# Optimization experiments

Measured on AMD Instinct MI355X. Metric: run time of the kernel, lower is better.

## Reference

```python
import jax, jax.numpy as jnp
import numpy as np

THRESHOLD = 0.5

def _conv(x, w, b):
    y = jax.lax.conv_general_dilated(x, w, (1, 1), 'SAME',
                                     dimension_numbers=('NCHW', 'OIHW', 'NCHW'))
    return y + b[None, :, None, None]

def _gather2d(img, iy, ix):
    # img [B,C,H,W], iy/ix [B,h,w] int -> [B,C,h,w]
    return jax.vmap(lambda im, y, x: im[:, y, x])(img, iy, ix)

def _grid_sample_bilinear(img, grid):
    # torch F.grid_sample(mode='bilinear', padding_mode='border', align_corners=False)
    # img [B,C,H,W], grid [B,h,w,2] with (x,y) in [-1,1]
    B, C, H, W = img.shape
    x = (grid[..., 0] + 1.0) * (W * 0.5) - 0.5
    y = (grid[..., 1] + 1.0) * (H * 0.5) - 0.5
    x0 = jnp.floor(x); y0 = jnp.floor(y)
    wx = (x - x0)[:, None, :, :]; wy = (y - y0)[:, None, :, :]
    x0i = jnp.clip(x0.astype(jnp.int32), 0, W - 1)
    x1i = jnp.clip(x0.astype(jnp.int32) + 1, 0, W - 1)
    y0i = jnp.clip(y0.astype(jnp.int32), 0, H - 1)
    y1i = jnp.clip(y0.astype(jnp.int32) + 1, 0, H - 1)
    v00 = _gather2d(img, y0i, x0i); v01 = _gather2d(img, y0i, x1i)
    v10 = _gather2d(img, y1i, x0i); v11 = _gather2d(img, y1i, x1i)
    return (v00 * (1 - wx) * (1 - wy) + v01 * wx * (1 - wy)
            + v10 * (1 - wx) * wy + v11 * wx * wy)

def _encoder(lr, w_in, b_in, res_w, res_b):
    x = _conv(lr, w_in, b_in)
    for i in range(res_w.shape[0]):  # small fixed layer count
        r = _conv(jax.nn.relu(_conv(x, res_w[i, 0], res_b[i, 0])), res_w[i, 1], res_b[i, 1])
        x = x + r
    return x  # [B,64,Hl,Wl]

def _make_inp(feat, coord, cell):
    # nearest-sampled feature + relative coord + scaled cell (LIIF-style make_inp)
    B, C, Hl, Wl = feat.shape
    y = (coord[..., 0] + 1.0) * (Hl * 0.5) - 0.5
    x = (coord[..., 1] + 1.0) * (Wl * 0.5) - 0.5
    iyn = jnp.clip(jnp.floor(y + 0.5).astype(jnp.int32), 0, Hl - 1)
    ixn = jnp.clip(jnp.floor(x + 0.5).astype(jnp.int32), 0, Wl - 1)
    fs = _gather2d(feat, iyn, ixn).transpose(0, 2, 3, 1)  # [B,h,w,C]
    cy = (2.0 * iyn + 1.0) / Hl - 1.0
    cx = (2.0 * ixn + 1.0) / Wl - 1.0
    rel = jnp.stack([(coord[..., 0] - cy) * Hl, (coord[..., 1] - cx) * Wl], axis=-1)
    cell_s = cell * jnp.array([Hl, Wl], dtype=cell.dtype)
    return jnp.concatenate([fs, rel, cell_s], axis=-1)  # [B,h,w,C+4]

def setup_inputs() -> dict:
    key = jax.random.key(0)
    ks = jax.random.split(key, 16)
    B, Hl, Wl, h, w, C = 2, 96, 96, 384, 384, 64
    lr = jax.random.normal(ks[0], (B, 3, Hl, Wl), jnp.float32)
    ys = (jnp.arange(h, dtype=jnp.float32) + 0.5) / h * 2.0 - 1.0
    xs = (jnp.arange(w, dtype=jnp.float32) + 0.5) / w * 2.0 - 1.0
    gy, gx = jnp.meshgrid(ys, xs, indexing='ij')
    coord = jnp.broadcast_to(jnp.stack([gy, gx], -1), (B, h, w, 2))  # (y,x)
    cell = jnp.broadcast_to(jnp.array([2.0 / h, 2.0 / w], jnp.float32), (B, h, w, 2))
    def lin(k, fan_in, shape):
        return jax.random.normal(k, shape, jnp.float32) / np.sqrt(fan_in)
    D = C + 4  # 68
    return {
        'lr': lr, 'coord': coord, 'cell': cell,
        'enc_w_in': jax.random.normal(ks[1], (C, 3, 3, 3), jnp.float32) * 0.05,
        'enc_b_in': jnp.zeros((C,), jnp.float32),
        'enc_res_w': jax.random.normal(ks[2], (4, 2, C, C, 3, 3), jnp.float32) * 0.02,
        'enc_res_b': jnp.zeros((4, 2, C), jnp.float32),
        'cls_w1': lin(ks[3], D, (D, 64)), 'cls_b1': jnp.zeros((64,), jnp.float32),
        'cls_w2': lin(ks[4], 64, (64, 2)), 'cls_b2': jnp.zeros((2,), jnp.float32),
        'lw1': lin(ks[5], D, (D, 64)), 'lb1': jnp.zeros((64,), jnp.float32),
        'lw2': lin(ks[6], 64, (64, 64)), 'lb2': jnp.zeros((64,), jnp.float32),
        'lw3': lin(ks[7], 64, (64, 3)), 'lb3': jnp.zeros((3,), jnp.float32),
        'hw1': lin(ks[8], D, (D, 256)), 'hb1': jnp.zeros((256,), jnp.float32),
        'hmid_w': lin(ks[9], 256, (2, 256, 256)), 'hmid_b': jnp.zeros((2, 256), jnp.float32),
        'hw_out': lin(ks[10], 256, (256, 3)), 'hb_out': jnp.zeros((3,), jnp.float32),
    }

def reference(lr, coord, cell, enc_w_in, enc_b_in, enc_res_w, enc_res_b,
              cls_w1, cls_b1, cls_w2, cls_b2,
              lw1, lb1, lw2, lb2, lw3, lb3,
              hw1, hb1, hmid_w, hmid_b, hw_out, hb_out):
    feat = _encoder(lr, enc_w_in, enc_b_in, enc_res_w, enc_res_b)
    inp = _make_inp(feat, coord, cell)  # [B,h,w,68]
    # classifier -> softmax difficulty gate
    logits = jax.nn.relu(inp @ cls_w1 + cls_b1) @ cls_w2 + cls_b2
    diff = jax.nn.softmax(logits, axis=-1)
    hard = diff[..., 1] > THRESHOLD  # [B,h,w]
    # light sampler (dense over all pixels; where-select == gather/scatter dispatch)
    pl = jax.nn.relu(inp @ lw1 + lb1)
    pl = jax.nn.relu(pl @ lw2 + lb2)
    pl = pl @ lw3 + lb3
    # heavy sampler
    ph = jax.nn.relu(inp @ hw1 + hb1)
    for i in range(hmid_w.shape[0]):
        ph = jax.nn.relu(ph @ hmid_w[i] + hmid_b[i])
    ph = ph @ hw_out + hb_out
    pred = jnp.where(hard[..., None], ph, pl)  # [B,h,w,3]
    pred = pred.transpose(0, 3, 1, 2)  # [B,3,h,w]
    pred = pred + _grid_sample_bilinear(lr, coord[..., ::-1])  # coord.flip(-1) -> (x,y)
    ratio_easy = jnp.mean(1.0 - hard.astype(jnp.float32))
    return (pred, ratio_easy)
```

## Files before the change

### kernel.cpp

```cpp
#include <hip/hip_runtime.h>

#define HL 96
#define WL 96
#define HO 384
#define WO 384
#define NPIX (2*HO*WO)
#define FEAT_ELEMS ((size_t)2*64*HL*WL)
#define PLANE (HL*WL)

typedef unsigned short us4 __attribute__((ext_vector_type(4)));
typedef unsigned short us8 __attribute__((ext_vector_type(8)));
typedef __bf16         b8  __attribute__((ext_vector_type(8)));
typedef float          f32x4 __attribute__((ext_vector_type(4)));

__device__ __forceinline__ unsigned short f2b(float x) {
  unsigned u = __builtin_bit_cast(unsigned, x);
  unsigned r = (u + 0x7FFFu + ((u >> 16) & 1u)) >> 16;
  return (unsigned short)r;
}

__device__ __forceinline__ f32x4 MF(us8 a, us8 b, f32x4 c) {
  return __builtin_amdgcn_mfma_f32_16x16x32_bf16(
      __builtin_bit_cast(b8, a), __builtin_bit_cast(b8, b), c, 0, 0, 0);
}

template<int CIN, int COPT, bool RELU, bool RES>
__global__ __launch_bounds__(256) void conv_s_k(
    const float* __restrict__ in, const float* __restrict__ wP,
    const float* __restrict__ bias, const float* __restrict__ res,
    float* __restrict__ out)
{
  const int t   = threadIdx.x;
  const int p   = blockIdx.x * 256 + t;
  const int co0 = blockIdx.y * COPT;
  const int b   = blockIdx.z;
  const int x   = p % WL;
  const bool xl = (x == 0), xr = (x == WL - 1);

  float acc[COPT];
  #pragma unroll
  for (int j = 0; j < COPT; ++j) acc[j] = bias[co0 + j];

  int  ic[3]; bool yv[3];
  int  im[3], ip[3];
  #pragma unroll
  for (int ky = 0; ky < 3; ++ky) {
    int pr = p + (ky - 1) * WL;
    yv[ky] = ((unsigned)pr < (unsigned)PLANE);
    ic[ky] = yv[ky] ? pr : 0;
    im[ky] = ic[ky] - 1; if (im[ky] < 0) im[ky] = 0;
    ip[ky] = ic[ky] + 1; if (ip[ky] > PLANE - 1) ip[ky] = PLANE - 1;
  }

  const float* inb = in + (size_t)b * CIN * PLANE;

  #pragma unroll 2
  for (int ci = 0; ci < CIN; ++ci) {
    const float* pl = inb + (size_t)ci * PLANE;
    #pragma unroll
    for (int ky = 0; ky < 3; ++ky) {
      float am = pl[im[ky]];
      float a0 = pl[ic[ky]];
      float ap = pl[ip[ky]];
      if (!yv[ky]) { am = 0.f; a0 = 0.f; ap = 0.f; }
      if (xl) am = 0.f;
      if (xr) ap = 0.f;
      const float* wrow = wP + (size_t)(ci * 9 + ky * 3) * 64 + co0;
      #pragma unroll
      for (int j = 0; j < COPT; ++j) acc[j] += am * wrow[j];
      #pragma unroll
      for (int j = 0; j < COPT; ++j) acc[j] += a0 * wrow[64 + j];
      #pragma unroll
      for (int j = 0; j < COPT; ++j) acc[j] += ap * wrow[128 + j];
    }
  }

  size_t ob = ((size_t)b * 64 + co0) * PLANE + p;
  #pragma unroll
  for (int j = 0; j < COPT; ++j) {
    float v = acc[j];
    if (RELU) v = fmaxf(v, 0.f);
    if (RES)  v += res[ob + (size_t)j * PLANE];
    out[ob + (size_t)j * PLANE] = v;
  }
}

__device__ __forceinline__ void prep_bf16(const float* __restrict__ src,
    unsigned short* __restrict__ dst, int K, int N, int Kp, int i)
{
  int n = i / Kp, k = i - n * Kp;
  float v = (k < K && n < N) ? src[(size_t)k * N + n] : 0.f;
  dst[i] = f2b(v);
}
__device__ __forceinline__ void prep_conv(const float* __restrict__ src,
    float* __restrict__ dst, int cin, int i)
{
  int co = i % 64; int r = i / 64;
  int ci = r / 9, tap = r % 9;
  dst[i] = src[((size_t)co * cin + ci) * 9 + tap];
}

#define PREP_TOTAL 467648
__global__ __launch_bounds__(256) void prep_all_k(
    const float* __restrict__ lw1, const float* __restrict__ lw2,
    const float* __restrict__ lw3, const float* __restrict__ hw1,
    const float* __restrict__ hmw, const float* __restrict__ hwo,
    const float* __restrict__ enc_w_in, const float* __restrict__ enc_rw,
    unsigned short* __restrict__ lw1T, unsigned short* __restrict__ lw2T,
    unsigned short* __restrict__ lw3T, unsigned short* __restrict__ hw1T,
    unsigned short* __restrict__ hm0T, unsigned short* __restrict__ hm1T,
    unsigned short* __restrict__ hwoT, float* __restrict__ cwIn,
    float* __restrict__ cwRes)
{
  int i = blockIdx.x * 256 + threadIdx.x;
  if (i >= PREP_TOTAL) return;
  if (i < 6144)  { prep_bf16(lw1, lw1T, 68, 64, 96, i);    return; } i -= 6144;
  if (i < 4096)  { prep_bf16(lw2, lw2T, 64, 64, 64, i);    return; } i -= 4096;
  if (i < 1024)  { prep_bf16(lw3, lw3T, 64, 3, 64, i);     return; } i -= 1024;
  if (i < 24576) { prep_bf16(hw1, hw1T, 68, 256, 96, i);   return; } i -= 24576;
  if (i < 65536) { prep_bf16(hmw, hm0T, 256, 256, 256, i); return; } i -= 65536;
  if (i < 65536) { prep_bf16(hmw + 65536, hm1T, 256, 256, 256, i); return; } i -= 65536;
  if (i < 4096)  { prep_bf16(hwo, hwoT, 256, 3, 256, i);   return; } i -= 4096;
  if (i < 1728)  { prep_conv(enc_w_in, cwIn, 3, i);        return; } i -= 1728;
  int l = i / 36864, r = i % 36864;
  prep_conv(enc_rw + (size_t)l * 36864, cwRes + (size_t)l * 36864, 64, r);
}

__global__ __launch_bounds__(256) void nchw_to_nhwc_k(const float* __restrict__ in,
                                                      float* __restrict__ out)
{
  __shared__ float s[64][65];
  const int b = blockIdx.y;
  const int pix0 = blockIdx.x * 64;
  const int t = threadIdx.x;
  #pragma unroll
  for (int cc = 0; cc < 16; ++cc) {
    int co = cc * 4 + (t >> 6);
    int px = t & 63;
    s[px][co] = in[((size_t)b * 64 + co) * PLANE + pix0 + px];
  }
  __syncthreads();
  #pragma unroll
  for (int pp = 0; pp < 16; ++pp) {
    int px = pp * 4 + (t >> 6);
    int co = t & 63;
    out[((size_t)b * PLANE + pix0 + px) * 64 + co] = s[px][co];
  }
}

template<int NT, int KT>
__device__ __forceinline__ void mfma_compute(
    const unsigned short* __restrict__ aBase, int AS,
    const unsigned short* __restrict__ WT, int Kpad,
    int n0, int lane, f32x4 (&acc)[4][NT])
{
  const int lr = lane & 15;
  const int lc = lane >> 4;
  #pragma unroll
  for (int m = 0; m < 4; ++m)
    #pragma unroll
    for (int j = 0; j < NT; ++j) acc[m][j] = (f32x4){0.f, 0.f, 0.f, 0.f};

  const unsigned short* aP = aBase + lr * AS + lc * 8;
  const unsigned short* bP = WT + (size_t)(n0 + lr) * Kpad + lc * 8;

  constexpr int KCH = (KT >= 4) ? 4 : KT;
  #pragma unroll
  for (int kc = 0; kc < KT; kc += KCH) {
    us8 breg[KCH][NT];
    #pragma unroll
    for (int kk = 0; kk < KCH; ++kk)
      #pragma unroll
      for (int j = 0; j < NT; ++j)
        breg[kk][j] = *(const us8*)(bP + (size_t)j * 16 * Kpad + (kc + kk) * 32);
    #pragma unroll
    for (int kc2 = 0; kc2 < KCH; ++kc2) {
      us8 a0[4];
      #pragma unroll
      for (int m = 0; m < 4; ++m)
        a0[m] = *(const us8*)(aP + (m * 16) * AS + (kc + kc2) * 32);
      #pragma unroll
      for (int m = 0; m < 4; ++m)
        #pragma unroll
        for (int j = 0; j < NT; ++j)
          acc[m][j] = MF(a0[m], breg[kc2][j], acc[m][j]);
    }
  }
}

template<int NT, bool RELU>
__device__ __forceinline__ void mfma_store(
    const f32x4 (&acc)[4][NT], const float* __restrict__ bias,
    unsigned short* __restrict__ dBase, int DS, int dCol0, int n0, int lane)
{
  const int lr = lane & 15;
  const int lc = lane >> 4;
  #pragma unroll
  for (int j = 0; j < NT; ++j) {
    int n = n0 + j * 16 + lr;
    float bv = bias[n];
    #pragma unroll
    for (int m = 0; m < 4; ++m)
      #pragma unroll
      for (int r = 0; r < 4; ++r) {
        float v = acc[m][j][r] + bv;
        if (RELU) v = fmaxf(v, 0.f);
        dBase[(m * 16 + lc * 4 + r) * DS + dCol0 + n] = f2b(v);
      }
  }
}

template<int KT>
__device__ __forceinline__ void mfma_out3w(
    const unsigned short* __restrict__ aBase, int AS,
    const unsigned short* __restrict__ WT, int Kpad,
    const float* __restrict__ bias, float (*dst)[4], int mtile, int lane)
{
  const int lr = lane & 15;
  const int lc = lane >> 4;
  f32x4 acc = (f32x4){0.f, 0.f, 0.f, 0.f};
  const unsigned short* aP = aBase + (mtile * 16 + lr) * AS + lc * 8;
  const unsigned short* bP = WT + (size_t)lr * Kpad + lc * 8;

  constexpr int KCH = (KT >= 4) ? 4 : KT;
  #pragma unroll
  for (int kc = 0; kc < KT; kc += KCH) {
    us8 breg[KCH];
    #pragma unroll
    for (int kk = 0; kk < KCH; ++kk)
      breg[kk] = *(const us8*)(bP + (kc + kk) * 32);
    #pragma unroll
    for (int kk = 0; kk < KCH; ++kk) {
      us8 a = *(const us8*)(aP + (kc + kk) * 32);
      acc = MF(a, breg[kk], acc);
    }
  }
  if (lr < 3) {
    float bv = bias[lr];
    #pragma unroll
    for (int r = 0; r < 4; ++r)
      dst[mtile * 16 + lc * 4 + r][lr] = acc[r] + bv;
  }
}

__device__ __forceinline__ void nearest_idx(float gy, float gx, int& iy, int& ix)
{
  float fy = (gy + 1.f) * (HL * 0.5f) - 0.5f;
  float fx = (gx + 1.f) * (WL * 0.5f) - 0.5f;
  iy = min(max((int)floorf(fy + 0.5f), 0), HL - 1);
  ix = min(max((int)floorf(fx + 0.5f), 0), WL - 1);
}

__device__ __forceinline__ float bilinear_lr(const float* __restrict__ lrimg,
                                             int b, int ch, float gy, float gx)
{
  float x = (gx + 1.f) * (WL * 0.5f) - 0.5f;
  float y = (gy + 1.f) * (HL * 0.5f) - 0.5f;
  float xf = floorf(x), yf = floorf(y);
  float wx = x - xf, wy = y - yf;
  int x0i = min(max((int)xf,     0), WL - 1);
  int x1i = min(max((int)xf + 1, 0), WL - 1);
  int y0i = min(max((int)yf,     0), HL - 1);
  int y1i = min(max((int)yf + 1, 0), HL - 1);
  const float* img = lrimg + ((size_t)b * 3 + ch) * PLANE;
  float v00 = img[y0i * WL + x0i], v01 = img[y0i * WL + x1i];
  float v10 = img[y1i * WL + x0i], v11 = img[y1i * WL + x1i];
  return v00 * (1.f - wx) * (1.f - wy) + v01 * wx * (1.f - wy)
       + v10 * (1.f - wx) * wy + v11 * wx * wy;
}

template<int JB>
__device__ __forceinline__ void cls_block2(
    const float* __restrict__ fpA, const float* __restrict__ fpB,
    const float4& eA, const float4& eB,
    const float* __restrict__ cw1, const float* __restrict__ cb1,
    const float* __restrict__ cw2, int j0,
    float& l0a, float& l1a, float& l0b, float& l1b)
{
  float accA[JB], accB[JB];
  #pragma unroll
  for (int j = 0; j < JB; ++j) { accA[j] = cb1[j0 + j]; accB[j] = accA[j]; }
  #pragma unroll 4
  for (int kq = 0; kq < 16; ++kq) {
    float4 a4A = *(const float4*)(fpA + kq * 4);
    float4 a4B = *(const float4*)(fpB + kq * 4);
    float avA[4] = {a4A.x, a4A.y, a4A.z, a4A.w};
    float avB[4] = {a4B.x, a4B.y, a4B.z, a4B.w};
    #pragma unroll
    for (int kk = 0; kk < 4; ++kk) {
      const float* wr = cw1 + (size_t)(kq * 4 + kk) * 64 + j0;
      float aA = avA[kk], aB = avB[kk];
      #pragma unroll
      for (int j = 0; j < JB; ++j) { accA[j] += aA * wr[j]; accB[j] += aB * wr[j]; }
    }
  }
  {
    const float* wr = cw1 + (size_t)64 * 64 + j0;
    #pragma unroll
    for (int j = 0; j < JB; ++j) { accA[j] += eA.x * wr[j]; accB[j] += eB.x * wr[j]; }
    wr += 64;
    #pragma unroll
    for (int j = 0; j < JB; ++j) { accA[j] += eA.y * wr[j]; accB[j] += eB.y * wr[j]; }
    wr += 64;
    #pragma unroll
    for (int j = 0; j < JB; ++j) { accA[j] += eA.z * wr[j]; accB[j] += eB.z * wr[j]; }
    wr += 64;
    #pragma unroll
    for (int j = 0; j < JB; ++j) { accA[j] += eA.w * wr[j]; accB[j] += eB.w * wr[j]; }
  }
  #pragma unroll
  for (int j = 0; j < JB; ++j) {
    float hA = fmaxf(accA[j], 0.f);
    float hB = fmaxf(accB[j], 0.f);
    float w0 = cw2[(j0 + j) * 2 + 0], w1 = cw2[(j0 + j) * 2 + 1];
    l0a += hA * w0; l1a += hA * w1;
    l0b += hB * w0; l1b += hB * w1;
  }
}

__global__ __launch_bounds__(256, 4) void cls_gate2_k(
    const float* __restrict__ featT, const float* __restrict__ coord,
    const float* __restrict__ cell,
    const float* __restrict__ cw1, const float* __restrict__ cb1,
    const float* __restrict__ cw2, const float* __restrict__ cb2,
    int* __restrict__ counters, unsigned* __restrict__ easyList,
    unsigned* __restrict__ hardList)
{
  const int T  = blockIdx.x * 256 + threadIdx.x;
  const int gA = T * 2, gB = gA + 1;

  int bA = gA / (HO * WO);
  float gyA = coord[(size_t)gA * 2 + 0];
  float gxA = coord[(size_t)gA * 2 + 1];
  int iyA, ixA; nearest_idx(gyA, gxA, iyA, ixA);
  const float* fpA = featT + (((size_t)bA * PLANE) + iyA * WL + ixA) * 64;
  float4 eA;
  { float cy = (2.f * iyA + 1.f) / HL - 1.f;
    float cx = (2.f * ixA + 1.f) / WL - 1.f;
    eA.x = (gyA - cy) * HL; eA.y = (gxA - cx) * WL;
    eA.z = cell[(size_t)gA * 2 + 0] * HL; eA.w = cell[(size_t)gA * 2 + 1] * WL; }

  int bB = gB / (HO * WO);
  float gyB = coord[(size_t)gB * 2 + 0];
  float gxB = coord[(size_t)gB * 2 + 1];
  int iyB, ixB; nearest_idx(gyB, gxB, iyB, ixB);
  const float* fpB = featT + (((size_t)bB * PLANE) + iyB * WL + ixB) * 64;
  float4 eB;
  { float cy = (2.f * iyB + 1.f) / HL - 1.f;
    float cx = (2.f * ixB + 1.f) / WL - 1.f;
    eB.x = (gyB - cy) * HL; eB.y = (gxB - cx) * WL;
    eB.z = cell[(size_t)gB * 2 + 0] * HL; eB.w = cell[(size_t)gB * 2 + 1] * WL; }

  float l0a = cb2[0], l1a = cb2[1];
  float l0b = cb2[0], l1b = cb2[1];
  cls_block2<32>(fpA, fpB, eA, eB, cw1, cb1, cw2, 0,  l0a, l1a, l0b, l1b);
  cls_block2<32>(fpA, fpB, eA, eB, cw1, cb1, cw2, 32, l0a, l1a, l0b, l1b);
  bool hardA = (l1a > l0a);
  bool hardB = (l1b > l0b);

  unsigned long long mh0 = __ballot(hardA);
  unsigned long long mh1 = __ballot(hardB);
  int lane = threadIdx.x & 63;
  int nh0 = __popcll(mh0), nh1 = __popcll(mh1);
  int nh = nh0 + nh1;
  int baseH = 0, baseE = 0;
  if (lane == 0) {
    baseH = atomicAdd(&counters[1], nh);
    baseE = atomicAdd(&counters[0], 128 - nh);
  }
  baseH = __shfl(baseH, 0);
  baseE = __shfl(baseE, 0);
  unsigned long long below = (1ull << lane) - 1ull;
  int hbA = __popcll(mh0 & below);
  int hbB = nh0 + __popcll(mh1 & below);
  int ebA = lane - hbA;
  int ebB = (64 - nh0) + (lane - __popcll(mh1 & below));
  if (hardA) hardList[baseH + hbA] = (unsigned)gA;
  else       easyList[baseE + ebA] = (unsigned)gA;
  if (hardB) hardList[baseH + hbB] = (unsigned)gB;
  else       easyList[baseE + ebB] = (unsigned)gB;
}

__device__ __forceinline__ void build_inp_row(
    const float* __restrict__ featT, const float* __restrict__ coord,
    const float* __restrict__ cell, unsigned g, int p, int q8,
    unsigned short (*sInpB)[104])
{
  int b = g / (HO * WO);
  float gy = coord[(size_t)g * 2 + 0];
  float gx = coord[(size_t)g * 2 + 1];
  int iy, ix; nearest_idx(gy, gx, iy, ix);
  const float* fpt = featT + (((size_t)b * PLANE) + iy * WL + ix) * 64 + q8 * 8;
  float4 u0 = *(const float4*)fpt;
  float4 u1 = *(const float4*)(fpt + 4);
  us8 pk;
  pk[0]=f2b(u0.x); pk[1]=f2b(u0.y); pk[2]=f2b(u0.z); pk[3]=f2b(u0.w);
  pk[4]=f2b(u1.x); pk[5]=f2b(u1.y); pk[6]=f2b(u1.z); pk[7]=f2b(u1.w);
  *(us8*)&sInpB[p][q8 * 8] = pk;
  if (q8 == 0) {
    float cy = (2.f * iy + 1.f) / HL - 1.f;
    float cx = (2.f * ix + 1.f) / WL - 1.f;
    float e0 = (gy - cy) * HL, e1 = (gx - cx) * WL;
    float e2 = cell[(size_t)g * 2 + 0] * HL, e3 = cell[(size_t)g * 2 + 1] * WL;
    us4 pe; pe[0]=f2b(e0); pe[1]=f2b(e1); pe[2]=f2b(e2); pe[3]=f2b(e3);
    *(us4*)&sInpB[p][64] = pe;
  }
  if (q8 == 1) {
    us4 z = (us4){0,0,0,0};
    #pragma unroll
    for (int c = 0; c < 9; ++c) *(us4*)&sInpB[p][68 + c * 4] = z;
  }
}

__global__ __launch_bounds__(256, 4) void light_k(
    const float* __restrict__ featT, const float* __restrict__ coord,
    const float* __restrict__ cell,  const float* __restrict__ lrimg,
    const float* __restrict__ lb1, const float* __restrict__ lb2,
    const float* __restrict__ lb3,
    const unsigned short* __restrict__ lw1T, const unsigned short* __restrict__ lw2T,
    const unsigned short* __restrict__ lw3T,
    const int* __restrict__ counters, const unsigned* __restrict__ list,
    float* __restrict__ out)
{
  const int nE = counters[0];
  const int g0 = blockIdx.x * 64;
  if (g0 >= nE) return;

  __shared__ unsigned short sInpB[64][104];
  __shared__ unsigned short sL1[64][72];
  __shared__ unsigned short sL2[64][72];
  __shared__ float sP[64][4];
  __shared__ unsigned sIdx[64];

  const int t = threadIdx.x, lane = t & 63, w = t >> 6;

  {
    const int p = t >> 2, q = t & 3;
    int i = g0 + p; if (i > nE - 1) i = nE - 1;
    unsigned g = list[i];
    if (q == 0) sIdx[p] = g;
    build_inp_row(featT, coord, cell, g, p, q * 2,     sInpB);
    build_inp_row(featT, coord, cell, g, p, q * 2 + 1, sInpB);
  }
  __syncthreads();

  { f32x4 acc[4][1];
    mfma_compute<1, 3>(&sInpB[0][0], 104, lw1T, 96, w * 16, lane, acc);
    mfma_store<1, true>(acc, lb1, &sL1[0][0], 72, 0, w * 16, lane); }
  __syncthreads();
  { f32x4 acc[4][1];
    mfma_compute<1, 2>(&sL1[0][0], 72, lw2T, 64, w * 16, lane, acc);
    mfma_store<1, true>(acc, lb2, &sL2[0][0], 72, 0, w * 16, lane); }
  __syncthreads();
  mfma_out3w<2>(&sL2[0][0], 72, lw3T, 64, lb3, sP, w, lane);
  __syncthreads();

  if (t < 192) {
    int p = t / 3, ch = t % 3;
    int i = g0 + p;
    if (i < nE) {
      unsigned g = sIdx[p];
      int b = g / (HO * WO);
      int rem = g % (HO * WO);
      int oy = rem / WO, ox = rem % WO;
      float gy = coord[(size_t)g * 2 + 0];
      float gx = coord[(size_t)g * 2 + 1];
      float v = bilinear_lr(lrimg, b, ch, gy, gx);
      out[(((size_t)b * 3 + ch) * HO + oy) * WO + ox] = sP[p][ch] + v;
    }
  }
}

__global__ __launch_bounds__(512, 4) void heavy_k(
    const float* __restrict__ featT, const float* __restrict__ coord,
    const float* __restrict__ cell,  const float* __restrict__ lrimg,
    const float* __restrict__ hb1, const float* __restrict__ hmb,
    const float* __restrict__ hbo,
    const unsigned short* __restrict__ hw1T, const unsigned short* __restrict__ hm0T,
    const unsigned short* __restrict__ hm1T, const unsigned short* __restrict__ hwoT,
    const int* __restrict__ counters, const unsigned* __restrict__ list,
    float* __restrict__ out)
{
  const int nH = counters[1];
  const int g0 = blockIdx.x * 64;
  if (g0 >= nH) return;

  __shared__ unsigned short sAct[64][264];
  __shared__ unsigned short sInpB[64][104];
  __shared__ float sP[64][4];
  __shared__ unsigned sIdx[64];

  const int t = threadIdx.x, lane = t & 63, w = t >> 6;

  {
    const int p = t >> 3, q = t & 7;
    int i = g0 + p; if (i > nH - 1) i = nH - 1;
    unsigned g = list[i];
    if (q == 0) sIdx[p] = g;
    build_inp_row(featT, coord, cell, g, p, q, sInpB);
  }
  __syncthreads();

  { f32x4 acc[4][2];
    mfma_compute<2, 3>(&sInpB[0][0], 104, hw1T, 96, w * 32, lane, acc);
    mfma_store<2, true>(acc, hb1, &sAct[0][0], 264, 0, w * 32, lane); }
  __syncthreads();
  { f32x4 acc[4][2];
    mfma_compute<2, 8>(&sAct[0][0], 264, hm0T, 256, w * 32, lane, acc);
    __syncthreads();
    mfma_store<2, true>(acc, hmb, &sAct[0][0], 264, 0, w * 32, lane); }
  __syncthreads();
  { f32x4 acc[4][2];
    mfma_compute<2, 8>(&sAct[0][0], 264, hm1T, 256, w * 32, lane, acc);
    __syncthreads();
    mfma_store<2, true>(acc, hmb + 256, &sAct[0][0], 264, 0, w * 32, lane); }
  __syncthreads();
  if (w < 4) mfma_out3w<8>(&sAct[0][0], 264, hwoT, 256, hbo, sP, w, lane);
  __syncthreads();

  if (t < 192) {
    int p = t / 3, ch = t % 3;
    int i = g0 + p;
    if (i < nH) {
      unsigned g = sIdx[p];
      int b = g / (HO * WO);
      int rem = g % (HO * WO);
      int oy = rem / WO, ox = rem % WO;
      float gy = coord[(size_t)g * 2 + 0];
      float gx = coord[(size_t)g * 2 + 1];
      float v = bilinear_lr(lrimg, b, ch, gy, gx);
      out[(((size_t)b * 3 + ch) * HO + oy) * WO + ox] = sP[p][ch] + v;
    }
  }
}

__global__ void finalize_k(const int* __restrict__ counters, float* __restrict__ out)
{
  out[(size_t)NPIX * 3] = (float)(counters[0]) / (float)NPIX;
}

extern "C" void kernel_launch(void* const* d_in, const int* in_sizes, int n_in,
                              void* d_out, int out_size, void* d_ws, size_t ws_size,
                              hipStream_t stream)
{
  const float* lr       = (const float*)d_in[0];
  const float* coord    = (const float*)d_in[1];
  const float* cell     = (const float*)d_in[2];
  const float* enc_w_in = (const float*)d_in[3];
  const float* enc_b_in = (const float*)d_in[4];
  const float* enc_rw   = (const float*)d_in[5];
  const float* enc_rb   = (const float*)d_in[6];
  const float* cw1      = (const float*)d_in[7];
  const float* cb1      = (const float*)d_in[8];
  const float* cw2      = (const float*)d_in[9];
  const float* cb2      = (const float*)d_in[10];
  const float* lw1      = (const float*)d_in[11];
  const float* lb1      = (const float*)d_in[12];
  const float* lw2      = (const float*)d_in[13];
  const float* lb2      = (const float*)d_in[14];
  const float* lw3      = (const float*)d_in[15];
  const float* lb3      = (const float*)d_in[16];
  const float* hw1      = (const float*)d_in[17];
  const float* hb1      = (const float*)d_in[18];
  const float* hmw      = (const float*)d_in[19];
  const float* hmb      = (const float*)d_in[20];
  const float* hwo      = (const float*)d_in[21];
  const float* hbo      = (const float*)d_in[22];
  float* out = (float*)d_out;

  char* ws = (char*)d_ws;
  float* xA    = (float*)(ws + 1024);
  float* tmp   = xA  + FEAT_ELEMS;
  float* xB    = tmp + FEAT_ELEMS;
  float* featT = tmp;
  unsigned short* wb = (unsigned short*)(xB + FEAT_ELEMS);
  unsigned short* lw1T = wb;
  unsigned short* lw2T = lw1T + 64*96;
  unsigned short* lw3T = lw2T + 64*64;
  unsigned short* hw1T = lw3T + 16*64;
  unsigned short* hm0T = hw1T + 256*96;
  unsigned short* hm1T = hm0T + 65536;
  unsigned short* hwoT = hm1T + 65536;
  const size_t nb16 = 64*96 + 64*64 + 16*64 + 256*96 + 2*65536 + 16*256;
  float* cwIn  = (float*)(wb + nb16);
  float* cwRes = cwIn + 1728;
  size_t need = 1024 + 3 * FEAT_ELEMS * sizeof(float)
              + nb16 * 2 + (1728 + 8 * 36864) * sizeof(float);
  if (ws_size < need) return;

  int*      counters = (int*)xB;
  unsigned* easyList = (unsigned*)(xB + 16);
  unsigned* hardList = easyList + NPIX;

  prep_all_k<<<(PREP_TOTAL + 255) / 256, 256, 0, stream>>>(
      lw1, lw2, lw3, hw1, hmw, hwo, enc_w_in, enc_rw,
      lw1T, lw2T, lw3T, hw1T, hm0T, hm1T, hwoT, cwIn, cwRes);

  dim3 cgrid(36, 16, 2);
  conv_s_k<3, 4, false, false><<<cgrid, 256, 0, stream>>>(lr, cwIn, enc_b_in, nullptr, xA);

  float* cur = xA; float* oth = xB;
  for (int i = 0; i < 4; ++i) {
    const float* wp0 = cwRes + (size_t)(2 * i)     * 36864;
    const float* wp1 = cwRes + (size_t)(2 * i + 1) * 36864;
    const float* b0 = enc_rb + i * 128;
    const float* b1 = b0 + 64;
    conv_s_k<64, 4, true,  false><<<cgrid, 256, 0, stream>>>(cur, wp0, b0, nullptr, tmp);
    conv_s_k<64, 4, false, true ><<<cgrid, 256, 0, stream>>>(tmp, wp1, b1, cur, oth);
    float* sw2 = cur; cur = oth; oth = sw2;
  }

  nchw_to_nhwc_k<<<dim3(144, 2), 256, 0, stream>>>(cur, featT);

  hipMemsetAsync(counters, 0, 16, stream);

  cls_gate2_k<<<NPIX / 512, 256, 0, stream>>>(featT, coord, cell,
      cw1, cb1, cw2, cb2, counters, easyList, hardList);

  light_k<<<NPIX / 64, 256, 0, stream>>>(featT, coord, cell, lr,
      lb1, lb2, lb3, lw1T, lw2T, lw3T, counters, easyList, out);

  heavy_k<<<NPIX / 64, 512, 0, stream>>>(featT, coord, cell, lr,
      hb1, hmb, hbo, hw1T, hm0T, hm1T, hwoT, counters, hardList, out);

  finalize_k<<<1, 1, 0, stream>>>(counters, out);
}
```

Measured before the change: 623.3 us.

## Fuse light and heavy samplers into one launch; add compact-weight residual conv

Merges the light and heavy MLP kernels into one launch. The first half of the grid handles hard pixels and the second half handles easy pixels, so the two paths can overlap and one launch with its tail is removed. It also adds a residual-block conv kernel that stages only the 4 output channels' weights per block in shared memory (a group-interleaved layout produced by a new prep routine), instead of the full 64-channel weight row. Light blocks now run at 512 threads with half the waves idle, which may reduce occupancy for the easy path.

```diff
diff --git a/kernel.cpp b/kernel.cpp
--- a/kernel.cpp
+++ b/kernel.cpp
@@ -7,6 +7,7 @@
 #define NPIX (2*HO*WO)
 #define FEAT_ELEMS ((size_t)2*64*HL*WL)
 #define PLANE (HL*WL)
+#define HGRID (NPIX/64)
 
 typedef unsigned short us4 __attribute__((ext_vector_type(4)));
 typedef unsigned short us8 __attribute__((ext_vector_type(8)));
@@ -85,6 +86,76 @@
   }
 }
 
+template<bool RELU, bool RES>
+__global__ __launch_bounds__(256) void conv_lw_k(
+    const float* __restrict__ in, const float* __restrict__ wG,
+    const float* __restrict__ bias, const float* __restrict__ res,
+    float* __restrict__ out)
+{
+  __shared__ float sw[576 * 4];
+
+  const int t   = threadIdx.x;
+  const int p   = blockIdx.x * 256 + t;
+  const int co0 = blockIdx.y * 4;
+  const int b   = blockIdx.z;
+  const int x   = p % WL;
+  const bool xl = (x == 0), xr = (x == WL - 1);
+
+  {
+    const float4* s4 = (const float4*)(wG + (size_t)blockIdx.y * 2304);
+    float4* d4 = (float4*)sw;
+    for (int i = t; i < 576; i += 256) d4[i] = s4[i];
+  }
+
+  float acc[4];
+  #pragma unroll
+  for (int j = 0; j < 4; ++j) acc[j] = bias[co0 + j];
+
+  int  ic[3]; bool yv[3];
+  int  im[3], ip[3];
+  #pragma unroll
+  for (int ky = 0; ky < 3; ++ky) {
+    int pr = p + (ky - 1) * WL;
+    yv[ky] = ((unsigned)pr < (unsigned)PLANE);
+    ic[ky] = yv[ky] ? pr : 0;
+    im[ky] = ic[ky] - 1; if (im[ky] < 0) im[ky] = 0;
+    ip[ky] = ic[ky] + 1; if (ip[ky] > PLANE - 1) ip[ky] = PLANE - 1;
+  }
+
+  const float* inb = in + (size_t)b * 64 * PLANE;
+  __syncthreads();
+
+  #pragma unroll 2
+  for (int ci = 0; ci < 64; ++ci) {
+    const float* pl = inb + (size_t)ci * PLANE;
+    #pragma unroll
+    for (int ky = 0; ky < 3; ++ky) {
+      float am = pl[im[ky]];
+      float a0 = pl[ic[ky]];
+      float ap = pl[ip[ky]];
+      if (!yv[ky]) { am = 0.f; a0 = 0.f; ap = 0.f; }
+      if (xl) am = 0.f;
+      if (xr) ap = 0.f;
+      const float* wrow = &sw[(ci * 9 + ky * 3) * 4];
+      #pragma unroll
+      for (int j = 0; j < 4; ++j) acc[j] += am * wrow[j];
+      #pragma unroll
+      for (int j = 0; j < 4; ++j) acc[j] += a0 * wrow[4 + j];
+      #pragma unroll
+      for (int j = 0; j < 4; ++j) acc[j] += ap * wrow[8 + j];
+    }
+  }
+
+  size_t ob = ((size_t)b * 64 + co0) * PLANE + p;
+  #pragma unroll
+  for (int j = 0; j < 4; ++j) {
+    float v = acc[j];
+    if (RELU) v = fmaxf(v, 0.f);
+    if (RES)  v += res[ob + (size_t)j * PLANE];
+    out[ob + (size_t)j * PLANE] = v;
+  }
+}
+
 __device__ __forceinline__ void prep_bf16(const float* __restrict__ src,
     unsigned short* __restrict__ dst, int K, int N, int Kp, int i)
 {
@@ -98,6 +169,17 @@
   int co = i % 64; int r = i / 64;
   int ci = r / 9, tap = r % 9;
   dst[i] = src[((size_t)co * cin + ci) * 9 + tap];
+}
+__device__ __forceinline__ void prep_conv2(const float* __restrict__ src,
+    float* __restrict__ dst, int i)
+{
+  int j  = i & 3;
+  int t2 = i >> 2;
+  int cg = t2 / 576;
+  int r  = t2 - cg * 576;
+  int ci = r / 9, tap = r - ci * 9;
+  int co = cg * 4 + j;
+  dst[i] = src[((size_t)co * 64 + ci) * 9 + tap];
 }
 
 #define PREP_TOTAL 467648
@@ -123,7 +205,7 @@
   if (i < 4096)  { prep_bf16(hwo, hwoT, 256, 3, 256, i);   return; } i -= 4096;
   if (i < 1728)  { prep_conv(enc_w_in, cwIn, 3, i);        return; } i -= 1728;
   int l = i / 36864, r = i % 36864;
-  prep_conv(enc_rw + (size_t)l * 36864, cwRes + (size_t)l * 36864, 64, r);
+  prep_conv2(enc_rw + (size_t)l * 36864, cwRes + (size_t)l * 36864, r);
 }
 
 __global__ __launch_bounds__(256) void nchw_to_nhwc_k(const float* __restrict__ in,
@@ -412,124 +494,120 @@
   }
 }
 
-__global__ __launch_bounds__(256, 4) void light_k(
+__global__ __launch_bounds__(512, 4) void ml_k(
     const float* __restrict__ featT, const float* __restrict__ coord,
     const float* __restrict__ cell,  const float* __restrict__ lrimg,
     const float* __restrict__ lb1, const float* __restrict__ lb2,
     const float* __restrict__ lb3,
     const unsigned short* __restrict__ lw1T, const unsigned short* __restrict__ lw2T,
     const unsigned short* __restrict__ lw3T,
-    const int* __restrict__ counters, const unsigned* __restrict__ list,
-    float* __restrict__ out)
-{
-  const int nE = counters[0];
-  const int g0 = blockIdx.x * 64;
-  if (g0 >= nE) return;
-
-  __shared__ unsigned short sInpB[64][104];
-  __shared__ unsigned short sL1[64][72];
-  __shared__ unsigned short sL2[64][72];
-  __shared__ float sP[64][4];
-  __shared__ unsigned sIdx[64];
-
-  const int t = threadIdx.x, lane = t & 63, w = t >> 6;
-
-  {
-    const int p = t >> 2, q = t & 3;
-    int i = g0 + p; if (i > nE - 1) i = nE - 1;
-    unsigned g = list[i];
-    if (q == 0) sIdx[p] = g;
-    build_inp_row(featT, coord, cell, g, p, q * 2,     sInpB);
-    build_inp_row(featT, coord, cell, g, p, q * 2 + 1, sInpB);
-  }
-  __syncthreads();
-
-  { f32x4 acc[4][1];
-    mfma_compute<1, 3>(&sInpB[0][0], 104, lw1T, 96, w * 16, lane, acc);
-    mfma_store<1, true>(acc, lb1, &sL1[0][0], 72, 0, w * 16, lane); }
-  __syncthreads();
-  { f32x4 acc[4][1];
-    mfma_compute<1, 2>(&sL1[0][0], 72, lw2T, 64, w * 16, lane, acc);
-    mfma_store<1, true>(acc, lb2, &sL2[0][0], 72, 0, w * 16, lane); }
-  __syncthreads();
-  mfma_out3w<2>(&sL2[0][0], 72, lw3T, 64, lb3, sP, w, lane);
-  __syncthreads();
-
-  if (t < 192) {
-    int p = t / 3, ch = t % 3;
-    int i = g0 + p;
-    if (i < nE) {
-      unsigned g = sIdx[p];
-      int b = g / (HO * WO);
-      int rem = g % (HO * WO);
-      int oy = rem / WO, ox = rem % WO;
-      float gy = coord[(size_t)g * 2 + 0];
-      float gx = coord[(size_t)g * 2 + 1];
-      float v = bilinear_lr(lrimg, b, ch, gy, gx);
-      out[(((size_t)b * 3 + ch) * HO + oy) * WO + ox] = sP[p][ch] + v;
-    }
-  }
-}
-
-__global__ __launch_bounds__(512, 4) void heavy_k(
-    const float* __restrict__ featT, const float* __restrict__ coord,
-    const float* __restrict__ cell,  const float* __restrict__ lrimg,
     const float* __restrict__ hb1, const float* __restrict__ hmb,
     const float* __restrict__ hbo,
     const unsigned short* __restrict__ hw1T, const unsigned short* __restrict__ hm0T,
     const unsigned short* __restrict__ hm1T, const unsigned short* __restrict__ hwoT,
-    const int* __restrict__ counters, const unsigned* __restrict__ list,
+    const int* __restrict__ counters,
+    const unsigned* __restrict__ easyList, const unsigned* __restrict__ hardList,
     float* __restrict__ out)
 {
-  const int nH = counters[1];
-  const int g0 = blockIdx.x * 64;
-  if (g0 >= nH) return;
-
-  __shared__ unsigned short sAct[64][264];
+  __shared__ unsigned short sBuf[64 * 264];
   __shared__ unsigned short sInpB[64][104];
   __shared__ float sP[64][4];
   __shared__ unsigned sIdx[64];
 
   const int t = threadIdx.x, lane = t & 63, w = t >> 6;
-
-  {
-    const int p = t >> 3, q = t & 7;
-    int i = g0 + p; if (i > nH - 1) i = nH - 1;
-    unsigned g = list[i];
-    if (q == 0) sIdx[p] = g;
-    build_inp_row(featT, coord, cell, g, p, q, sInpB);
-  }
-  __syncthreads();
-
-  { f32x4 acc[4][2];
-    mfma_compute<2, 3>(&sInpB[0][0], 104, hw1T, 96, w * 32, lane, acc);
-    mfma_store<2, true>(acc, hb1, &sAct[0][0], 264, 0, w * 32, lane); }
-  __syncthreads();
-  { f32x4 acc[4][2];
-    mfma_compute<2, 8>(&sAct[0][0], 264, hm0T, 256, w * 32, lane, acc);
-    __syncthreads();
-    mfma_store<2, true>(acc, hmb, &sAct[0][0], 264, 0, w * 32, lane); }
-  __syncthreads();
-  { f32x4 acc[4][2];
-    mfma_compute<2, 8>(&sAct[0][0], 264, hm1T, 256, w * 32, lane, acc);
-    __syncthreads();
-    mfma_store<2, true>(acc, hmb + 256, &sAct[0][0], 264, 0, w * 32, lane); }
-  __syncthreads();
-  if (w < 4) mfma_out3w<8>(&sAct[0][0], 264, hwoT, 256, hbo, sP, w, lane);
-  __syncthreads();
-
-  if (t < 192) {
-    int p = t / 3, ch = t % 3;
-    int i = g0 + p;
-    if (i < nH) {
-      unsigned g = sIdx[p];
-      int b = g / (HO * WO);
-      int rem = g % (HO * WO);
-      int oy = rem / WO, ox = rem % WO;
-      float gy = coord[(size_t)g * 2 + 0];
-      float gx = coord[(size_t)g * 2 + 1];
-      float v = bilinear_lr(lrimg, b, ch, gy, gx);
-      out[(((size_t)b * 3 + ch) * HO + oy) * WO + ox] = sP[p][ch] + v;
+  const bool isH = (blockIdx.x < HGRID);
+
+  if (isH) {
+    const int nH = counters[1];
+    const int g0 = blockIdx.x * 64;
+    if (g0 >= nH) return;
+    unsigned short (*sAct)[264] = (unsigned short (*)[264])sBuf;
+
+    {
+      const int p = t >> 3, q = t & 7;
+      int i = g0 + p; if (i > nH - 1) i = nH - 1;
+      unsigned g = hardList[i];
+      if (q == 0) sIdx[p] = g;
+      build_inp_row(featT, coord, cell, g, p, q, sInpB);
+    }
+    __syncthreads();
+
+    { f32x4 acc[4][2];
+      mfma_compute<2, 3>(&sInpB[0][0], 104, hw1T, 96, w * 32, lane, acc);
+      mfma_store<2, true>(acc, hb1, &sAct[0][0], 264, 0, w * 32, lane); }
+    __syncthreads();
+    { f32x4 acc[4][2];
+      mfma_compute<2, 8>(&sAct[0][0], 264, hm0T, 256, w * 32, lane, acc);
+      __syncthreads();
+      mfma_store<2, true>(acc, hmb, &sAct[0][0], 264, 0, w * 32, lane); }
+    __syncthreads();
+    { f32x4 acc[4][2];
+      mfma_compute<2, 8>(&sAct[0][0], 264, hm1T, 256, w * 32, lane, acc);
+      __syncthreads();
+      mfma_store<2, true>(acc, hmb + 256, &sAct[0][0], 264, 0, w * 32, lane); }
+    __syncthreads();
+    if (w < 4) mfma_out3w<8>(&sAct[0][0], 264, hwoT, 256, hbo, sP, w, lane);
+    __syncthreads();
+
+    if (t < 192) {
+      int p = t / 3, ch = t % 3;
+      int i = g0 + p;
+      if (i < nH) {
+        unsigned g = sIdx[p];
+        int b = g / (HO * WO);
+        int rem = g % (HO * WO);
+        int oy = rem / WO, ox = rem % WO;
+        float gy = coord[(size_t)g * 2 + 0];
+        float gx = coord[(size_t)g * 2 + 1];
+        float v = bilinear_lr(lrimg, b, ch, gy, gx);
+        out[(((size_t)b * 3 + ch) * HO + oy) * WO + ox] = sP[p][ch] + v;
+      }
+    }
+  } else {
+    const int nE = counters[0];
+    const int g0 = (blockIdx.x - HGRID) * 64;
+    if (g0 >= nE) return;
+    unsigned short* sL1 = sBuf;
+    unsigned short* sL2 = sBuf + 64 * 72;
+
+    if (t < 256) {
+      const int p = t >> 2, q = t & 3;
+      int i = g0 + p; if (i > nE - 1) i = nE - 1;
+      unsigned g = easyList[i];
+      if (q == 0) sIdx[p] = g;
+      build_inp_row(featT, coord, cell, g, p, q * 2,     sInpB);
+      build_inp_row(featT, coord, cell, g, p, q * 2 + 1, sInpB);
+    }
+    __syncthreads();
+
+    if (w < 4) {
+      f32x4 acc[4][1];
+      mfma_compute<1, 3>(&sInpB[0][0], 104, lw1T, 96, w * 16, lane, acc);
+      mfma_store<1, true>(acc, lb1, sL1, 72, 0, w * 16, lane);
+    }
+    __syncthreads();
+    if (w < 4) {
+      f32x4 acc[4][1];
+      mfma_compute<1, 2>(sL1, 72, lw2T, 64, w * 16, lane, acc);
+      mfma_store<1, true>(acc, lb2, sL2, 72, 0, w * 16, lane);
+    }
+    __syncthreads();
+    if (w < 4) mfma_out3w<2>(sL2, 72, lw3T, 64, lb3, sP, w, lane);
+    __syncthreads();
+
+    if (t < 192) {
+      int p = t / 3, ch = t % 3;
+      int i = g0 + p;
+      if (i < nE) {
+        unsigned g = sIdx[p];
+        int b = g / (HO * WO);
+        int rem = g % (HO * WO);
+        int oy = rem / WO, ox = rem % WO;
+        float gy = coord[(size_t)g * 2 + 0];
+        float gx = coord[(size_t)g * 2 + 1];
+        float v = bilinear_lr(lrimg, b, ch, gy, gx);
+        out[(((size_t)b * 3 + ch) * HO + oy) * WO + ox] = sP[p][ch] + v;
+      }
     }
   }
 }
@@ -605,8 +683,8 @@
     const float* wp1 = cwRes + (size_t)(2 * i + 1) * 36864;
     const float* b0 = enc_rb + i * 128;
     const float* b1 = b0 + 64;
-    conv_s_k<64, 4, true,  false><<<cgrid, 256, 0, stream>>>(cur, wp0, b0, nullptr, tmp);
-    conv_s_k<64, 4, false, true ><<<cgrid, 256, 0, stream>>>(tmp, wp1, b1, cur, oth);
+    conv_lw_k<true,  false><<<cgrid, 256, 0, stream>>>(cur, wp0, b0, nullptr, tmp);
+    conv_lw_k<false, true ><<<cgrid, 256, 0, stream>>>(tmp, wp1, b1, cur, oth);
     float* sw2 = cur; cur = oth; oth = sw2;
   }
 
@@ -617,11 +695,10 @@
   cls_gate2_k<<<NPIX / 512, 256, 0, stream>>>(featT, coord, cell,
       cw1, cb1, cw2, cb2, counters, easyList, hardList);
 
-  light_k<<<NPIX / 64, 256, 0, stream>>>(featT, coord, cell, lr,
-      lb1, lb2, lb3, lw1T, lw2T, lw3T, counters, easyList, out);
-
-  heavy_k<<<NPIX / 64, 512, 0, stream>>>(featT, coord, cell, lr,
-      hb1, hmb, hbo, hw1T, hm0T, hm1T, hwoT, counters, hardList, out);
+  ml_k<<<2 * HGRID, 512, 0, stream>>>(featT, coord, cell, lr,
+      lb1, lb2, lb3, lw1T, lw2T, lw3T,
+      hb1, hmb, hbo, hw1T, hm0T, hm1T, hwoT,
+      counters, easyList, hardList, out);
 
   finalize_k<<<1, 1, 0, stream>>>(counters, out);
 }
```

New measurement: 604.9 us, median of 2. -3.0%, faster.
